# Performance work log

Measured on AMD Instinct MI355X. Metric: run time of the kernel, lower is better.

Reference implementation:

```python
import jax, jax.numpy as jnp
import numpy as np

DIM = 1024
S_SIZE = 512
M_SIZE = 4096
L_SIZE = 8192
MERGE_THRESHOLD = 0.98
L_ALPHA = 0.1
K_PROMOTE = max(1, S_SIZE // 4)  # torch: min(len(candidates), max(1, s_size//4)); candidates >> s_size here


def _l2norm(x, axis=-1):
    # F.normalize(p=2) with eps clamp
    return x / jnp.maximum(jnp.linalg.norm(x, axis=axis, keepdims=True), 1e-12)


def _update(processed_tokens, s_memory, m_memory, l_memory, m_utility, l_utility, wq, bq, wk, bk, s_ptr):
    cand = processed_tokens.reshape(-1, DIM)
    # --- S tier: scatter top-k-norm candidates into ring buffer (vectorized; K<=S so slots distinct) ---
    norms = jnp.linalg.norm(cand, axis=1)
    _, top_idx = jax.lax.top_k(norms, K_PROMOTE)
    pos = (s_ptr + jnp.arange(K_PROMOTE)) % S_SIZE
    s_mem = s_memory.at[pos].set(cand[top_idx])
    s_ptr_new = (s_ptr + K_PROMOTE) % S_SIZE
    # --- promotion attention (1 head, only attn weights used): pick best short-term slot ---
    q = l_memory.mean(axis=0) @ wq.T + bq                      # [dim]
    kproj = s_mem @ wk.T + bk                                  # [S, dim]
    attn = jax.nn.softmax(kproj @ q / jnp.sqrt(jnp.asarray(DIM, cand.dtype)))
    best_s_idx = jnp.argmax(attn)
    candidate = s_mem[best_s_idx]                              # [dim]

    # --- M tier: promote / merge / replace ---
    def not_full(mm, mu):
        ridx = jnp.argmin(mu)
        return mm.at[ridx].set(candidate), mu.at[ridx].set(mu.mean() + 1e-5)

    def full(mm, mu):
        mm_norm = _l2norm(mm)
        sims = mm_norm @ _l2norm(candidate)                    # [M]
        msi = jnp.argmax(sims)
        sim_cand = sims[msi]

        def merge_with_candidate(mm, mu):
            merged = _l2norm((mm[msi] + candidate) / 2.0)
            return mm.at[msi].set(merged), mu.at[msi].set((mu[msi] + mu.mean()) / 2.0)

        def try_internal_merge(mm, mu):
            # most redundant pair: strict lower triangle of cosine sim matrix
            sim_mat = mm_norm @ mm_norm.T                      # [M, M]
            sim_mat = jnp.where(jnp.triu(jnp.ones((M_SIZE, M_SIZE), bool)), -1.0, sim_mat)
            flat = jnp.argmax(sim_mat)
            internal_sim = sim_mat.reshape(-1)[flat]
            idx1, idx2 = flat // M_SIZE, flat % M_SIZE

            def do_pair_merge(mm, mu):
                merged = _l2norm((mm[idx1] + mm[idx2]) / 2.0)
                mm2 = mm.at[idx1].set(merged).at[idx2].set(candidate)
                mu1 = mu.at[idx1].set((mu[idx1] + mu[idx2]) / 2.0)
                mu2 = mu1.at[idx2].set(mu1.mean() + 1e-5)      # torch recomputes mean after idx1 write
                return mm2, mu2

            def replace_weakest(mm, mu):
                li = jnp.argmin(mu)
                stronger = jnp.linalg.norm(candidate) > jnp.linalg.norm(mm[li])
                mm2 = jnp.where(stronger, mm.at[li].set(candidate), mm)
                mu2 = jnp.where(stronger, mu.at[li].set(mu.mean() + 1e-5), mu)
                return mm2, mu2

            return jax.lax.cond(internal_sim > MERGE_THRESHOLD, do_pair_merge, replace_weakest, mm, mu)

        return jax.lax.cond(sim_cand > MERGE_THRESHOLD, merge_with_candidate, try_internal_merge, mm, mu)

    is_m_full = ~jnp.any(m_utility == 0)
    m_mem, m_util = jax.lax.cond(is_m_full, full, not_full, m_memory, m_utility)
    # --- L tier: consolidate most-used M slot into least-used L slot ---
    mi = jnp.argmax(m_util)
    lj = jnp.argmin(l_utility)
    consolidated = (1.0 - L_ALPHA) * l_memory[lj] + L_ALPHA * m_mem[mi]
    l_mem = l_memory.at[lj].set(consolidated)
    l_util = l_utility.at[lj].set(l_utility.mean())            # mean of pre-write values
    return s_mem, m_mem, l_mem, m_util, l_util, s_ptr_new


def setup_inputs() -> dict:
    key = jax.random.key(0)
    ks = jax.random.split(key, 10)
    scale = 1.0 / np.sqrt(DIM)
    return {
        "processed_tokens": jax.random.normal(ks[0], (4, 4096, DIM), jnp.float32),
        "s_memory": jax.random.normal(ks[1], (S_SIZE, DIM), jnp.float32),
        "m_memory": jax.random.normal(ks[2], (M_SIZE, DIM), jnp.float32),
        "l_memory": jax.random.normal(ks[3], (L_SIZE, DIM), jnp.float32),
        "m_utility": jax.random.uniform(ks[4], (M_SIZE,), jnp.float32) + 0.01,  # >0 -> 'm full' branch
        "l_utility": jax.random.uniform(ks[5], (L_SIZE,), jnp.float32) + 0.01,
        "wq": jax.random.normal(ks[6], (DIM, DIM), jnp.float32) * scale,
        "bq": jnp.zeros((DIM,), jnp.float32),
        "wk": jax.random.normal(ks[7], (DIM, DIM), jnp.float32) * scale,
        "bk": jnp.zeros((DIM,), jnp.float32),
        "s_ptr": 0,
    }


def reference(processed_tokens, s_memory, m_memory, l_memory, m_utility, l_utility, wq, bq, wk, bk, s_ptr):
    return _update(processed_tokens, s_memory, m_memory, l_memory, m_utility, l_utility, wq, bq, wk, bk, s_ptr)
```

## Files before the change

kernel.cpp:

```cpp
#include <hip/hip_runtime.h>

#define DIMV 1024
#define SSZ 512
#define MSZ 4096
#define LSZ 8192
#define KPROM 128
#define NCAND 16384
#define NPAIR 528

typedef __attribute__((ext_vector_type(4))) float f32x4;
typedef __attribute__((ext_vector_type(4))) unsigned int u32x4;
typedef __attribute__((ext_vector_type(4))) unsigned short u16x4;
typedef __attribute__((ext_vector_type(8))) __bf16 bf16x8;

#define OUT_S 0ull
#define OUT_M 524288ull
#define OUT_L 4718592ull
#define OUT_MU 13107200ull
#define OUT_LU 13111296ull
#define OUT_SPTR 13119488ull

#define SC_BF16 0ull
#define SC_NORMS 2100000ull
#define SC_TOPIDX 2117000ull
#define SC_LPART 2120000ull
#define SC_RV 2260000ull
#define SC_LMEAN 2262000ull
#define SC_Q 2264000ull
#define SC_LOGITS 2413000ull
#define SC_BEST 2414000ull
#define SC_MNORM 2415000ull
#define SC_SIMS 2420000ull
#define SC_PPV 2425000ull
#define SC_PPI 2427000ull

__device__ __forceinline__ float wave_sum(float v) {
#pragma unroll
  for (int o = 32; o > 0; o >>= 1) v += __shfl_down(v, o, 64);
  return v;
}
__device__ __forceinline__ void wave_maxidx(float& v, int& i) {
#pragma unroll
  for (int o = 32; o > 0; o >>= 1) {
    float ov = __shfl_down(v, o, 64);
    int oi = __shfl_down(i, o, 64);
    if (ov > v || (ov == v && oi < i)) { v = ov; i = oi; }
  }
}
__device__ __forceinline__ void wave_minidx(float& v, int& i) {
#pragma unroll
  for (int o = 32; o > 0; o >>= 1) {
    float ov = __shfl_down(v, o, 64);
    int oi = __shfl_down(i, o, 64);
    if (ov < v || (ov == v && oi < i)) { v = ov; i = oi; }
  }
}
__device__ __forceinline__ unsigned short f2bf(float x) {
  unsigned u = __float_as_uint(x);
  return (unsigned short)((u + 0x7FFFu + ((u >> 16) & 1u)) >> 16);
}
__device__ __forceinline__ void gload16(const unsigned short* g, unsigned short* l) {
  __builtin_amdgcn_global_load_lds((const __attribute__((address_space(1))) unsigned int*)(g),
                                   (__attribute__((address_space(3))) unsigned int*)(l), 16, 0, 0);
}

__global__ void kA(const float* __restrict__ cand, const float* __restrict__ l_memory,
                   const float* __restrict__ m, float* __restrict__ norms,
                   float* __restrict__ lpart, unsigned short* __restrict__ mb,
                   float* __restrict__ mnorm) {
  int b = blockIdx.x, t = threadIdx.x, lane = t & 63, w = t >> 6;
  if (b < 128) {
    f32x4 a0 = {0.f, 0.f, 0.f, 0.f}, a1 = a0, a2 = a0, a3 = a0;
    const f32x4* base = (const f32x4*)(l_memory + (size_t)b * 64 * DIMV);
#pragma unroll 4
    for (int r = 0; r < 64; r += 4) {
      a0 += base[(r + 0) * 256 + t];
      a1 += base[(r + 1) * 256 + t];
      a2 += base[(r + 2) * 256 + t];
      a3 += base[(r + 3) * 256 + t];
    }
    f32x4 a = (a0 + a1) + (a2 + a3);
    ((f32x4*)(lpart + (size_t)b * DIMV))[t] = a;
  } else if (b < 1152) {
    int r0 = (b - 128) * 16 + w * 4;
    const f32x4* base4 = (const f32x4*)(cand + (size_t)r0 * DIMV);
    float s0 = 0.f, s1 = 0.f, s2 = 0.f, s3 = 0.f;
#pragma unroll
    for (int k = 0; k < 16; ++k) {
      f32x4 v = base4[k * 64 + lane];
      float d = v.x * v.x + v.y * v.y + v.z * v.z + v.w * v.w;
      if (k < 4) s0 += d;
      else if (k < 8) s1 += d;
      else if (k < 12) s2 += d;
      else s3 += d;
    }
    f32x4 sv = {s0, s1, s2, s3};
#pragma unroll
    for (int o = 32; o > 0; o >>= 1) {
      sv.x += __shfl_down(sv.x, o, 64);
      sv.y += __shfl_down(sv.y, o, 64);
      sv.z += __shfl_down(sv.z, o, 64);
      sv.w += __shfl_down(sv.w, o, 64);
    }
    if (lane == 0) {
      f32x4 o4 = {sqrtf(sv.x), sqrtf(sv.y), sqrtf(sv.z), sqrtf(sv.w)};
      *((f32x4*)(norms + r0)) = o4;
    }
  } else {
    int r0 = (b - 1152) * 16 + w * 4;
    const f32x4* base4 = (const f32x4*)(m + (size_t)r0 * DIMV);
    u16x4* mb4 = (u16x4*)(mb + (size_t)r0 * DIMV);
    float s0 = 0.f, s1 = 0.f, s2 = 0.f, s3 = 0.f;
#pragma unroll
    for (int k = 0; k < 16; ++k) {
      int i = k * 64 + lane;
      f32x4 v = base4[i];
      float d = v.x * v.x + v.y * v.y + v.z * v.z + v.w * v.w;
      if (k < 4) s0 += d;
      else if (k < 8) s1 += d;
      else if (k < 12) s2 += d;
      else s3 += d;
      u16x4 h;
      h.x = f2bf(v.x); h.y = f2bf(v.y); h.z = f2bf(v.z); h.w = f2bf(v.w);
      mb4[i] = h;
    }
    f32x4 sv = {s0, s1, s2, s3};
#pragma unroll
    for (int o = 32; o > 0; o >>= 1) {
      sv.x += __shfl_down(sv.x, o, 64);
      sv.y += __shfl_down(sv.y, o, 64);
      sv.z += __shfl_down(sv.z, o, 64);
      sv.w += __shfl_down(sv.w, o, 64);
    }
    if (lane == 0) {
      f32x4 o4 = {sqrtf(sv.x), sqrtf(sv.y), sqrtf(sv.z), sqrtf(sv.w)};
      *((f32x4*)(mnorm + r0)) = o4;
    }
  }
}

__device__ int scan_excl_1024(int v, int* sh, int* total) {
  int t = threadIdx.x;
  sh[t] = v;
  __syncthreads();
  for (int o = 1; o < 1024; o <<= 1) {
    int x = (t >= o) ? sh[t - o] : 0;
    __syncthreads();
    sh[t] += x;
    __syncthreads();
  }
  int incl = sh[t];
  *total = sh[1023];
  __syncthreads();
  return incl - v;
}

__global__ void kT(const float* __restrict__ norms, int* __restrict__ topidx,
                   const float* __restrict__ lpart, float* __restrict__ lmean) {
  int t = threadIdx.x;
  if (blockIdx.x == 1) {
    float s = 0.f;
    for (int p = 0; p < 128; ++p) s += lpart[(size_t)p * DIMV + t];
    lmean[t] = s * (1.f / 8192.f);
    return;
  }
  __shared__ int sh[1024];
  __shared__ int hist[256];
  __shared__ unsigned s_selkey[KPROM];
  __shared__ int s_selidx[KPROM];
  __shared__ int s_digit, s_sub;
  unsigned key[16];
#pragma unroll
  for (int j = 0; j < 16; ++j) key[j] = __float_as_uint(norms[t * 16 + j]);

  unsigned prefix = 0, himask = 0;
  int remaining = KPROM;
  for (int p = 24; p >= 0; p -= 8) {
    if (t < 256) hist[t] = 0;
    __syncthreads();
#pragma unroll
    for (int j = 0; j < 16; ++j)
      if ((key[j] & himask) == prefix) atomicAdd(&hist[(key[j] >> p) & 255], 1);
    __syncthreads();
    if (t < 256) sh[t] = hist[t];
    __syncthreads();
    for (int o = 1; o < 256; o <<= 1) {
      int x = (t < 256 && t + o < 256) ? sh[t + o] : 0;
      __syncthreads();
      if (t < 256) sh[t] += x;
      __syncthreads();
    }
    if (t < 256) {
      int sfex = (t < 255) ? sh[t + 1] : 0;
      if (sfex < remaining && remaining <= sh[t]) { s_digit = t; s_sub = sfex; }
    }
    __syncthreads();
    prefix |= ((unsigned)s_digit) << p;
    remaining -= s_sub;
    himask |= (0xFFu << p);
    __syncthreads();
  }
  unsigned T = prefix;

  int cgt = 0, ceq = 0;
#pragma unroll
  for (int j = 0; j < 16; ++j) { cgt += (key[j] > T); ceq += (key[j] == T); }
  int total_gt, total_eq;
  int sgt = scan_excl_1024(cgt, sh, &total_gt);
  int seq = scan_excl_1024(ceq, sh, &total_eq);
  int need_eq = KPROM - total_gt;
  int g = sgt, e = seq;
#pragma unroll
  for (int j = 0; j < 16; ++j) {
    if (key[j] > T) { s_selkey[g] = key[j]; s_selidx[g] = t * 16 + j; ++g; }
    else if (key[j] == T) {
      if (e < need_eq) { s_selkey[total_gt + e] = key[j]; s_selidx[total_gt + e] = t * 16 + j; }
      ++e;
    }
  }
  __syncthreads();
  if (t < KPROM) {
    unsigned mk = s_selkey[t];
    int mi = s_selidx[t];
    int rank = 0;
    for (int q2 = 0; q2 < KPROM; ++q2) {
      unsigned qk = s_selkey[q2];
      int qi = s_selidx[q2];
      rank += (qk > mk || (qk == mk && qi < mi)) ? 1 : 0;
    }
    topidx[rank] = mi;
  }
}

__global__ void kB(const float* __restrict__ cand, const float* __restrict__ s_memory,
                   const int* __restrict__ topidx, const int* __restrict__ s_ptr,
                   const float* __restrict__ wq, const float* __restrict__ bq,
                   const float* __restrict__ lmean, float* __restrict__ out_s,
                   float* __restrict__ out_sptr, float* __restrict__ qv) {
  int b = blockIdx.x, t = threadIdx.x;
  if (b < 512) {
    int sp = s_ptr[0];
    int k = (b - sp + SSZ) & (SSZ - 1);
    const float* src = (k < KPROM) ? (cand + (size_t)topidx[k] * DIMV) : (s_memory + (size_t)b * DIMV);
    ((f32x4*)(out_s + (size_t)b * DIMV))[t] = ((const f32x4*)src)[t];
    if (b == 0 && t == 0) out_sptr[0] = (float)((sp + KPROM) % SSZ);
  } else {
    int lane = t & 63, w = t >> 6;
    int d = (b - 512) * 4 + w;
    const f32x4* row = (const f32x4*)(wq + (size_t)d * DIMV);
    const f32x4* lm = (const f32x4*)lmean;
    float s = 0.f;
#pragma unroll
    for (int c = 0; c < 4; ++c) {
      f32x4 a = row[c * 64 + lane], bb = lm[c * 64 + lane];
      s += a.x * bb.x + a.y * bb.y + a.z * bb.z + a.w * bb.w;
    }
    s = wave_sum(s);
    if (lane == 0) qv[d] = s + bq[d];
  }
}

__global__ void kC(const float* __restrict__ wk, const float* __restrict__ qv,
                   float* __restrict__ rv) {
  int b = blockIdx.x, t = threadIdx.x;
  f32x4 a = {0.f, 0.f, 0.f, 0.f};
  for (int r = 0; r < 8; ++r) {
    float qd = qv[b * 8 + r];
    f32x4 v = ((const f32x4*)(wk + (size_t)(b * 8 + r) * DIMV))[t];
    a += v * qd;
  }
  atomicAdd(&rv[t * 4 + 0], a.x);
  atomicAdd(&rv[t * 4 + 1], a.y);
  atomicAdd(&rv[t * 4 + 2], a.z);
  atomicAdd(&rv[t * 4 + 3], a.w);
}

__global__ void kD(const float* __restrict__ out_s, const float* __restrict__ rv,
                   float* __restrict__ logits) {
  int lane = threadIdx.x & 63, w = threadIdx.x >> 6;
  int srow = blockIdx.x * 4 + w;
  const f32x4* a = (const f32x4*)(out_s + (size_t)srow * DIMV);
  const f32x4* b = (const f32x4*)rv;
  float s = 0.f;
#pragma unroll
  for (int c = 0; c < 4; ++c) {
    f32x4 x = a[c * 64 + lane], y = b[c * 64 + lane];
    s += x.x * y.x + x.y * y.y + x.z * y.z + x.w * y.w;
  }
  s = wave_sum(s);
  if (lane == 0) logits[srow] = s;
}

__global__ void kE(const float* __restrict__ logits, const float* __restrict__ out_s,
                   int* __restrict__ best, float* __restrict__ cnorm) {
  __shared__ float swv[4];
  __shared__ int swi[4];
  int t = threadIdx.x, lane = t & 63, w = t >> 6;
  float v0 = logits[t], v1 = logits[t + 256];
  float bv;
  int bidx;
  if (v1 > v0) { bv = v1; bidx = t + 256; } else { bv = v0; bidx = t; }
  wave_maxidx(bv, bidx);
  if (lane == 0) { swv[w] = bv; swi[w] = bidx; }
  __syncthreads();
  if (t == 0) {
    float a = swv[0]; int ai = swi[0];
    for (int i = 1; i < 4; ++i)
      if (swv[i] > a || (swv[i] == a && swi[i] < ai)) { a = swv[i]; ai = swi[i]; }
    best[0] = ai;
  }
  __syncthreads();
  int bi = best[0];
  f32x4 c4 = ((const f32x4*)(out_s + (size_t)bi * DIMV))[t];
  float s = c4.x * c4.x + c4.y * c4.y + c4.z * c4.z + c4.w * c4.w;
  s = wave_sum(s);
  __syncthreads();
  if (lane == 0) swv[w] = s;
  __syncthreads();
  if (t == 0) cnorm[0] = sqrtf(swv[0] + swv[1] + swv[2] + swv[3]);
}

__global__ __launch_bounds__(256, 3) void kG(const unsigned short* __restrict__ mb,
                                             const float* __restrict__ mnorm,
                                             const float* __restrict__ m,
                                             const float* __restrict__ out_s,
                                             const int* __restrict__ best,
                                             const float* __restrict__ cnorm,
                                             float* __restrict__ pv, int* __restrict__ pidx,
                                             float* __restrict__ sims) {
  int b = blockIdx.x, t = threadIdx.x, lane = t & 63, w = t >> 6;
  if (b >= NPAIR) {
    int row = (b - NPAIR) * 4 + w;
    const f32x4* mp = (const f32x4*)(m + (size_t)row * DIMV);
    const f32x4* cp = (const f32x4*)(out_s + (size_t)best[0] * DIMV);
    float sd = 0.f;
#pragma unroll
    for (int c = 0; c < 4; ++c) {
      int i = c * 64 + lane;
      f32x4 v = mp[i], u = cp[i];
      sd += v.x * u.x + v.y * u.y + v.z * u.z + v.w * u.w;
    }
    sd = wave_sum(sd);
    if (lane == 0) sims[row] = sd / (fmaxf(mnorm[row], 1e-12f) * fmaxf(cnorm[0], 1e-12f));
    return;
  }
  __shared__ unsigned short Ash[128 * 64];
  __shared__ unsigned short Bsh[128 * 64];
  __shared__ float spv[4];
  __shared__ int spi[4];

  int bs = (b & 7) * 66 + (b >> 3);
  int bi = (int)((sqrtf(8.f * (float)bs + 1.f) - 1.f) * 0.5f);
  while (bi * (bi + 1) / 2 > bs) --bi;
  while ((bi + 1) * (bi + 2) / 2 <= bs) ++bi;
  int bj = bs - bi * (bi + 1) / 2;
  int rowA0 = bi * 128, rowB0 = bj * 128;

  int wr = w >> 1, wc = w & 1;
  int rl = lane & 15, kq4 = lane >> 4;
  int swz = rl & 7;
  int subrow = lane >> 3, gg = lane & 7;
  int gsw = (gg ^ subrow) << 3;

  f32x4 acc[4][4];
  f32x4 z = {0.f, 0.f, 0.f, 0.f};
#pragma unroll
  for (int ti = 0; ti < 4; ++ti)
#pragma unroll
    for (int tj = 0; tj < 4; ++tj) acc[ti][tj] = z;

  for (int kc = 0; kc < DIMV; kc += 64) {
#pragma unroll
    for (int jj = 0; jj < 4; ++jj) {
      int rsub = w * 32 + jj * 8 + subrow;
      gload16(mb + (size_t)(rowA0 + rsub) * DIMV + kc + gsw, Ash + (w * 4 + jj) * 512);
      gload16(mb + (size_t)(rowB0 + rsub) * DIMV + kc + gsw, Bsh + (w * 4 + jj) * 512);
    }
    __syncthreads();
#pragma unroll
    for (int ks = 0; ks < 2; ++ks) {
      int co = (((ks * 4 + kq4) ^ swz) << 3);
      bf16x8 af[4], bfv[4];
#pragma unroll
      for (int ti = 0; ti < 4; ++ti)
        af[ti] = *(const bf16x8*)(Ash + (wr * 64 + ti * 16 + rl) * 64 + co);
#pragma unroll
      for (int tj = 0; tj < 4; ++tj)
        bfv[tj] = *(const bf16x8*)(Bsh + (wc * 64 + tj * 16 + rl) * 64 + co);
#pragma unroll
      for (int ti = 0; ti < 4; ++ti)
#pragma unroll
        for (int tj = 0; tj < 4; ++tj)
          acc[ti][tj] = __builtin_amdgcn_mfma_f32_16x16x32_bf16(af[ti], bfv[tj], acc[ti][tj], 0, 0, 0);
    }
    __syncthreads();
  }

  float ni[16], nj4[4];
#pragma unroll
  for (int ti = 0; ti < 4; ++ti)
#pragma unroll
    for (int r = 0; r < 4; ++r)
      ni[ti * 4 + r] = fmaxf(mnorm[rowA0 + wr * 64 + ti * 16 + kq4 * 4 + r], 1e-12f);
#pragma unroll
  for (int tj = 0; tj < 4; ++tj)
    nj4[tj] = fmaxf(mnorm[rowB0 + wc * 64 + tj * 16 + rl], 1e-12f);

  float bv = -3.402823466e38f;
  int bidx = 0x7FFFFFFF;
#pragma unroll
  for (int ti = 0; ti < 4; ++ti)
#pragma unroll
    for (int tj = 0; tj < 4; ++tj)
#pragma unroll
      for (int r = 0; r < 4; ++r) {
        int gi = rowA0 + wr * 64 + ti * 16 + kq4 * 4 + r;
        int gj = rowB0 + wc * 64 + tj * 16 + rl;
        if (gi > gj) {
          float s = acc[ti][tj][r] / (ni[ti * 4 + r] * nj4[tj]);
          int fi = gi * MSZ + gj;
          if (s > bv || (s == bv && fi < bidx)) { bv = s; bidx = fi; }
        }
      }
  wave_maxidx(bv, bidx);
  if (lane == 0) { spv[w] = bv; spi[w] = bidx; }
  __syncthreads();
  if (t == 0) {
    float a = spv[0]; int ai = spi[0];
    for (int i = 1; i < 4; ++i)
      if (spv[i] > a || (spv[i] == a && spi[i] < ai)) { a = spv[i]; ai = spi[i]; }
    pv[b] = a;
    pidx[b] = ai;
  }
}

__global__ void kH(const float* __restrict__ pv, const int* __restrict__ pidx,
                   const float* __restrict__ sims, const float* __restrict__ mu,
                   const float* __restrict__ mnorm, const float* __restrict__ cnorm,
                   const int* __restrict__ best, const float* __restrict__ lu,
                   float* __restrict__ out_mu, float* __restrict__ out_lu,
                   int* __restrict__ ws) {
  __shared__ float swv[16];
  __shared__ int swi[16];
  __shared__ float ssum[16];
  __shared__ int szf[16];
  __shared__ float s_res[2];
  __shared__ int s_resi[2];
  __shared__ int s_branch, s_i1, s_i2, s_lj;
  __shared__ float s_u1, s_u2, s_lmean;
  int t = threadIdx.x, lane = t & 63, w = t >> 6;

  float bv = -3.402823466e38f;
  int bidx = 0x7FFFFFFF;
  for (int i = t; i < NPAIR; i += 1024) {
    float v = pv[i];
    int fi = pidx[i];
    if (v > bv || (v == bv && fi < bidx)) { bv = v; bidx = fi; }
  }
  wave_maxidx(bv, bidx);
  if (lane == 0) { swv[w] = bv; swi[w] = bidx; }
  __syncthreads();
  if (t == 0) {
    float a = swv[0]; int ai = swi[0];
    for (int i = 1; i < 16; ++i)
      if (swv[i] > a || (swv[i] == a && swi[i] < ai)) { a = swv[i]; ai = swi[i]; }
    s_res[0] = a; s_resi[0] = ai;
  }
  __syncthreads();

  bv = -3.402823466e38f;
  bidx = 0x7FFFFFFF;
#pragma unroll
  for (int j = 0; j < 4; ++j) {
    int i = t * 4 + j;
    float v = sims[i];
    if (v > bv) { bv = v; bidx = i; }
  }
  wave_maxidx(bv, bidx);
  if (lane == 0) { swv[w] = bv; swi[w] = bidx; }
  __syncthreads();
  if (t == 0) {
    float a = swv[0]; int ai = swi[0];
    for (int i = 1; i < 16; ++i)
      if (swv[i] > a || (swv[i] == a && swi[i] < ai)) { a = swv[i]; ai = swi[i]; }
    s_res[1] = a; s_resi[1] = ai;
  }
  __syncthreads();

  float muv[4];
  float sum = 0.f, mnv = 3.402823466e38f;
  int mni = 0x7FFFFFFF, zf = 0;
#pragma unroll
  for (int j = 0; j < 4; ++j) {
    int i = t * 4 + j;
    float v = mu[i];
    muv[j] = v;
    sum += v;
    if (v < mnv) { mnv = v; mni = i; }
    if (v == 0.f) zf = 1;
  }
  sum = wave_sum(sum);
  wave_minidx(mnv, mni);
#pragma unroll
  for (int o = 32; o > 0; o >>= 1) zf |= __shfl_down(zf, o, 64);
  if (lane == 0) { ssum[w] = sum; swv[w] = mnv; swi[w] = mni; szf[w] = zf; }
  __syncthreads();
  if (t == 0) {
    float muSum = 0.f;
    int anyz = 0;
    float a = swv[0]; int li = swi[0];
    for (int i = 0; i < 16; ++i) {
      muSum += ssum[i];
      anyz |= szf[i];
      if (i > 0 && (swv[i] < a || (swv[i] == a && swi[i] < li))) { a = swv[i]; li = swi[i]; }
    }
    float muMean = muSum / 4096.f;
    float internal_sim = s_res[0];
    int iflat = s_resi[0];
    float sim_cand = s_res[1];
    int msi = s_resi[1];
    int branch, i1 = -1, i2 = -1;
    float u1 = 0.f, u2 = 0.f;
    if (anyz) {
      branch = 0; i1 = li; u1 = muMean + 1e-5f;
    } else if (sim_cand > 0.98f) {
      branch = 1; i1 = msi; u1 = (mu[msi] + muMean) * 0.5f;
    } else if (internal_sim > 0.98f) {
      branch = 2; i1 = iflat / MSZ; i2 = iflat - (iflat / MSZ) * MSZ;
      float o1 = mu[i1], o2 = mu[i2];
      u1 = (o1 + o2) * 0.5f;
      u2 = (muSum - o1 + u1) / 4096.f + 1e-5f;
    } else {
      if (cnorm[0] > mnorm[li]) { branch = 0; i1 = li; u1 = muMean + 1e-5f; }
      else branch = 4;
    }
    s_branch = branch; s_i1 = i1; s_i2 = i2; s_u1 = u1; s_u2 = u2;
    ws[2] = branch; ws[3] = i1; ws[4] = i2; ws[5] = best[0];
  }
  __syncthreads();

  int branch = s_branch, i1 = s_i1, i2 = s_i2;
  float u1 = s_u1, u2 = s_u2;
  bv = -3.402823466e38f;
  bidx = 0x7FFFFFFF;
#pragma unroll
  for (int j = 0; j < 4; ++j) {
    int i = t * 4 + j;
    float v = muv[j];
    if (branch != 4 && i == i1) v = u1;
    if (branch == 2 && i == i2) v = u2;
    out_mu[i] = v;
    if (v > bv) { bv = v; bidx = i; }
  }
  wave_maxidx(bv, bidx);
  __syncthreads();
  if (lane == 0) { swv[w] = bv; swi[w] = bidx; }
  __syncthreads();
  if (t == 0) {
    float a = swv[0]; int ai = swi[0];
    for (int i = 1; i < 16; ++i)
      if (swv[i] > a || (swv[i] == a && swi[i] < ai)) { a = swv[i]; ai = swi[i]; }
    ws[1] = ai;
  }

  float luv[8];
  sum = 0.f; mnv = 3.402823466e38f; mni = 0x7FFFFFFF;
#pragma unroll
  for (int j = 0; j < 8; ++j) {
    int i = t * 8 + j;
    float v = lu[i];
    luv[j] = v;
    sum += v;
    if (v < mnv) { mnv = v; mni = i; }
  }
  sum = wave_sum(sum);
  wave_minidx(mnv, mni);
  __syncthreads();
  if (lane == 0) { swv[w] = mnv; swi[w] = mni; ssum[w] = sum; }
  __syncthreads();
  if (t == 0) {
    float a = swv[0]; int ai = swi[0];
    float ls = 0.f;
    for (int i = 0; i < 16; ++i) {
      ls += ssum[i];
      if (i > 0 && (swv[i] < a || (swv[i] == a && swi[i] < ai))) { a = swv[i]; ai = swi[i]; }
    }
    s_lj = ai;
    s_lmean = ls / 8192.f;
    ws[0] = ai;
  }
  __syncthreads();
  int lj = s_lj;
  float lmv = s_lmean;
#pragma unroll
  for (int j = 0; j < 8; ++j) {
    int i = t * 8 + j;
    out_lu[i] = (i == lj) ? lmv : luv[j];
  }
}

__global__ void kI(const float* __restrict__ m, const float* __restrict__ l_memory,
                   const float* __restrict__ out_s, const int* __restrict__ ws,
                   float* __restrict__ out_m, float* __restrict__ out_l) {
  __shared__ float sred[4];
  int b = blockIdx.x, t = threadIdx.x, lane = t & 63, w = t >> 6;
  int lj = ws[0], mi = ws[1], branch = ws[2], i1 = ws[3], i2 = ws[4], best = ws[5];
  if (b < 1024) {
    int r0 = b * 4;
    bool special = (branch != 4) &&
                   ((i1 >= r0 && i1 < r0 + 4) || (branch == 2 && i2 >= r0 && i2 < r0 + 4));
    if (!special) {
      const f32x4* src = (const f32x4*)(m + (size_t)r0 * DIMV);
      f32x4* dst = (f32x4*)(out_m + (size_t)r0 * DIMV);
#pragma unroll
      for (int k = 0; k < 4; ++k) dst[k * 256 + t] = src[k * 256 + t];
      return;
    }
    for (int rr = 0; rr < 4; ++rr) {
      int row = r0 + rr;
      int mode = 0;
      if ((branch == 0 && row == i1) || (branch == 2 && row == i2)) mode = 1;
      else if (branch == 1 && row == i1) mode = 2;
      else if (branch == 2 && row == i1) mode = 3;
      f32x4* dst = (f32x4*)(out_m + (size_t)row * DIMV);
      if (mode == 0) {
        dst[t] = ((const f32x4*)(m + (size_t)row * DIMV))[t];
      } else if (mode == 1) {
        dst[t] = ((const f32x4*)(out_s + (size_t)best * DIMV))[t];
      } else {
        f32x4 a = ((const f32x4*)(m + (size_t)row * DIMV))[t];
        f32x4 bb = (mode == 2) ? ((const f32x4*)(out_s + (size_t)best * DIMV))[t]
                               : ((const f32x4*)(m + (size_t)i2 * DIMV))[t];
        f32x4 v = (a + bb) * 0.5f;
        float ss = v.x * v.x + v.y * v.y + v.z * v.z + v.w * v.w;
        ss = wave_sum(ss);
        if (lane == 0) sred[w] = ss;
        __syncthreads();
        float nrm = fmaxf(sqrtf(sred[0] + sred[1] + sred[2] + sred[3]), 1e-12f);
        __syncthreads();
        dst[t] = v / nrm;
      }
    }
  } else {
    int r0 = (b - 1024) * 4;
    bool special = (lj >= r0 && lj < r0 + 4);
    if (!special) {
      const f32x4* src = (const f32x4*)(l_memory + (size_t)r0 * DIMV);
      f32x4* dst = (f32x4*)(out_l + (size_t)r0 * DIMV);
#pragma unroll
      for (int k = 0; k < 4; ++k) dst[k * 256 + t] = src[k * 256 + t];
      return;
    }
    for (int rr = 0; rr < 4; ++rr) {
      int row = r0 + rr;
      f32x4 v = ((const f32x4*)(l_memory + (size_t)row * DIMV))[t];
      if (row == lj) {
        int mode = 0;
        if ((branch == 0 && mi == i1) || (branch == 2 && mi == i2)) mode = 1;
        else if (branch == 1 && mi == i1) mode = 2;
        else if (branch == 2 && mi == i1) mode = 3;
        f32x4 mv;
        if (mode == 0) {
          mv = ((const f32x4*)(m + (size_t)mi * DIMV))[t];
        } else if (mode == 1) {
          mv = ((const f32x4*)(out_s + (size_t)best * DIMV))[t];
        } else {
          f32x4 a = ((const f32x4*)(m + (size_t)mi * DIMV))[t];
          f32x4 bb = (mode == 2) ? ((const f32x4*)(out_s + (size_t)best * DIMV))[t]
                                 : ((const f32x4*)(m + (size_t)i2 * DIMV))[t];
          f32x4 vm = (a + bb) * 0.5f;
          float ss = vm.x * vm.x + vm.y * vm.y + vm.z * vm.z + vm.w * vm.w;
          ss = wave_sum(ss);
          if (lane == 0) sred[w] = ss;
          __syncthreads();
          float nrm = fmaxf(sqrtf(sred[0] + sred[1] + sred[2] + sred[3]), 1e-12f);
          __syncthreads();
          mv = vm / nrm;
        }
        v = v * 0.9f + mv * 0.1f;
      }
      ((f32x4*)(out_l + (size_t)row * DIMV))[t] = v;
    }
  }
}

extern "C" void kernel_launch(void* const* d_in, const int* in_sizes, int n_in,
                              void* d_out, int out_size, void* d_ws, size_t ws_size,
                              hipStream_t stream) {
  const float* cand = (const float*)d_in[0];
  const float* s_memory = (const float*)d_in[1];
  const float* m_memory = (const float*)d_in[2];
  const float* l_memory = (const float*)d_in[3];
  const float* m_utility = (const float*)d_in[4];
  const float* l_utility = (const float*)d_in[5];
  const float* wq = (const float*)d_in[6];
  const float* bq = (const float*)d_in[7];
  const float* wk = (const float*)d_in[8];
  const float* bk = (const float*)d_in[9];
  const int* s_ptr = (const int*)d_in[10];
  (void)bk;

  float* out = (float*)d_out;
  float* out_s = out + OUT_S;
  float* out_m = out + OUT_M;
  float* out_l = out + OUT_L;
  float* out_mu = out + OUT_MU;
  float* out_lu = out + OUT_LU;
  float* out_sptr = out + OUT_SPTR;

  float* lsc = out_l;
  unsigned short* mb = (unsigned short*)(lsc + SC_BF16);
  float* norms = lsc + SC_NORMS;
  int* topidx = (int*)(lsc + SC_TOPIDX);
  float* lpart = lsc + SC_LPART;
  float* rv = lsc + SC_RV;
  float* lmean = lsc + SC_LMEAN;
  float* qv = lsc + SC_Q;
  float* logits = lsc + SC_LOGITS;
  int* best = (int*)(lsc + SC_BEST);
  float* cnorm = lsc + SC_BEST + 1;
  float* mnorm = lsc + SC_MNORM;
  float* sims = lsc + SC_SIMS;
  float* pv = lsc + SC_PPV;
  int* pidx = (int*)(lsc + SC_PPI);
  int* wsctl = (int*)d_ws;

  hipMemsetAsync(rv, 0, 4096, stream);
  kA<<<1408, 256, 0, stream>>>(cand, l_memory, m_memory, norms, lpart, mb, mnorm);
  kT<<<2, 1024, 0, stream>>>(norms, topidx, lpart, lmean);
  kB<<<768, 256, 0, stream>>>(cand, s_memory, topidx, s_ptr, wq, bq, lmean, out_s, out_sptr, qv);
  kC<<<128, 256, 0, stream>>>(wk, qv, rv);
  kD<<<128, 256, 0, stream>>>(out_s, rv, logits);
  kE<<<1, 256, 0, stream>>>(logits, out_s, best, cnorm);
  kG<<<NPAIR + 1024, 256, 0, stream>>>(mb, mnorm, m_memory, out_s, best, cnorm, pv, pidx, sims);
  kH<<<1, 1024, 0, stream>>>(pv, pidx, sims, m_utility, mnorm, cnorm, best, l_utility,
                             out_mu, out_lu, wsctl);
  kI<<<3072, 256, 0, stream>>>(m_memory, l_memory, out_s, wsctl, out_m, out_l);
}
```

Before: 284.0 us.

## Fuse M/L passthrough copies into first streaming pass with nontemporal stores

```diff
diff --git a/kernel.cpp b/kernel.cpp
--- a/kernel.cpp
+++ b/kernel.cpp
@@ -20,19 +20,19 @@
 #define OUT_LU 13111296ull
 #define OUT_SPTR 13119488ull
 
+#define SCROWS 2080
 #define SC_BF16 0ull
-#define SC_NORMS 2100000ull
-#define SC_TOPIDX 2117000ull
-#define SC_LPART 2120000ull
-#define SC_RV 2260000ull
-#define SC_LMEAN 2262000ull
-#define SC_Q 2264000ull
-#define SC_LOGITS 2413000ull
-#define SC_BEST 2414000ull
-#define SC_MNORM 2415000ull
-#define SC_SIMS 2420000ull
-#define SC_PPV 2425000ull
-#define SC_PPI 2427000ull
+#define SC_NORMS 2097152ull
+#define SC_TOPIDX 2113536ull
+#define SC_RV 2113664ull
+#define SC_LSUM 2114688ull
+#define SC_QV 2115712ull
+#define SC_LOGITS 2116736ull
+#define SC_BEST 2117248ull
+#define SC_MNORM 2117264ull
+#define SC_SIMS 2121360ull
+#define SC_PPV 2125456ull
+#define SC_PPI 2125984ull
 
 __device__ __forceinline__ float wave_sum(float v) {
 #pragma unroll
@@ -59,6 +59,7 @@
   unsigned u = __float_as_uint(x);
   return (unsigned short)((u + 0x7FFFu + ((u >> 16) & 1u)) >> 16);
 }
+__device__ __forceinline__ void nts(f32x4* p, f32x4 v) { __builtin_nontemporal_store(v, p); }
 __device__ __forceinline__ void gload16(const unsigned short* g, unsigned short* l) {
   __builtin_amdgcn_global_load_lds((const __attribute__((address_space(1))) unsigned int*)(g),
                                    (__attribute__((address_space(3))) unsigned int*)(l), 16, 0, 0);
@@ -66,50 +67,40 @@
 
 __global__ void kA(const float* __restrict__ cand, const float* __restrict__ l_memory,
                    const float* __restrict__ m, float* __restrict__ norms,
-                   float* __restrict__ lpart, unsigned short* __restrict__ mb,
-                   float* __restrict__ mnorm) {
+                   float* __restrict__ lsum, unsigned short* __restrict__ mb,
+                   float* __restrict__ mnorm, float* __restrict__ out_m,
+                   float* __restrict__ out_l) {
   int b = blockIdx.x, t = threadIdx.x, lane = t & 63, w = t >> 6;
-  if (b < 128) {
+  if (b < 256) {
+    int r0 = b * 32;
+    const f32x4* base = (const f32x4*)l_memory + (size_t)r0 * 256;
+    f32x4* dst = (f32x4*)out_l + (size_t)r0 * 256;
+    bool wr = (r0 >= SCROWS);
     f32x4 a0 = {0.f, 0.f, 0.f, 0.f}, a1 = a0, a2 = a0, a3 = a0;
-    const f32x4* base = (const f32x4*)(l_memory + (size_t)b * 64 * DIMV);
-#pragma unroll 4
-    for (int r = 0; r < 64; r += 4) {
-      a0 += base[(r + 0) * 256 + t];
-      a1 += base[(r + 1) * 256 + t];
-      a2 += base[(r + 2) * 256 + t];
-      a3 += base[(r + 3) * 256 + t];
+#pragma unroll 2
+    for (int r = 0; r < 32; r += 4) {
+      f32x4 v0 = base[(r + 0) * 256 + t];
+      f32x4 v1 = base[(r + 1) * 256 + t];
+      f32x4 v2 = base[(r + 2) * 256 + t];
+      f32x4 v3 = base[(r + 3) * 256 + t];
+      if (wr) {
+        nts(&dst[(r + 0) * 256 + t], v0);
+        nts(&dst[(r + 1) * 256 + t], v1);
+        nts(&dst[(r + 2) * 256 + t], v2);
+        nts(&dst[(r + 3) * 256 + t], v3);
+      }
+      a0 += v0; a1 += v1; a2 += v2; a3 += v3;
     }
     f32x4 a = (a0 + a1) + (a2 + a3);
-    ((f32x4*)(lpart + (size_t)b * DIMV))[t] = a;
-  } else if (b < 1152) {
-    int r0 = (b - 128) * 16 + w * 4;
-    const f32x4* base4 = (const f32x4*)(cand + (size_t)r0 * DIMV);
-    float s0 = 0.f, s1 = 0.f, s2 = 0.f, s3 = 0.f;
-#pragma unroll
-    for (int k = 0; k < 16; ++k) {
-      f32x4 v = base4[k * 64 + lane];
-      float d = v.x * v.x + v.y * v.y + v.z * v.z + v.w * v.w;
-      if (k < 4) s0 += d;
-      else if (k < 8) s1 += d;
-      else if (k < 12) s2 += d;
-      else s3 += d;
-    }
-    f32x4 sv = {s0, s1, s2, s3};
-#pragma unroll
-    for (int o = 32; o > 0; o >>= 1) {
-      sv.x += __shfl_down(sv.x, o, 64);
-      sv.y += __shfl_down(sv.y, o, 64);
-      sv.z += __shfl_down(sv.z, o, 64);
-      sv.w += __shfl_down(sv.w, o, 64);
-    }
-    if (lane == 0) {
-      f32x4 o4 = {sqrtf(sv.x), sqrtf(sv.y), sqrtf(sv.z), sqrtf(sv.w)};
-      *((f32x4*)(norms + r0)) = o4;
-    }
-  } else {
-    int r0 = (b - 1152) * 16 + w * 4;
+    atomicAdd(&lsum[t * 4 + 0], a.x);
+    atomicAdd(&lsum[t * 4 + 1], a.y);
+    atomicAdd(&lsum[t * 4 + 2], a.z);
+    atomicAdd(&lsum[t * 4 + 3], a.w);
+  } else if (b < 512) {
+    int r0 = (b - 256) * 16 + w * 4;
     const f32x4* base4 = (const f32x4*)(m + (size_t)r0 * DIMV);
     u16x4* mb4 = (u16x4*)(mb + (size_t)r0 * DIMV);
+    f32x4* om4 = (f32x4*)(out_m + (size_t)r0 * DIMV);
     float s0 = 0.f, s1 = 0.f, s2 = 0.f, s3 = 0.f;
 #pragma unroll
     for (int k = 0; k < 16; ++k) {
@@ -123,6 +114,7 @@
       u16x4 h;
       h.x = f2bf(v.x); h.y = f2bf(v.y); h.z = f2bf(v.z); h.w = f2bf(v.w);
       mb4[i] = h;
+      nts(&om4[i], v);
     }
     f32x4 sv = {s0, s1, s2, s3};
 #pragma unroll
@@ -136,6 +128,31 @@
       f32x4 o4 = {sqrtf(sv.x), sqrtf(sv.y), sqrtf(sv.z), sqrtf(sv.w)};
       *((f32x4*)(mnorm + r0)) = o4;
     }
+  } else {
+    int r0 = (b - 512) * 16 + w * 4;
+    const f32x4* base4 = (const f32x4*)(cand + (size_t)r0 * DIMV);
+    float s0 = 0.f, s1 = 0.f, s2 = 0.f, s3 = 0.f;
+#pragma unroll
+    for (int k = 0; k < 16; ++k) {
+      f32x4 v = base4[k * 64 + lane];
+      float d = v.x * v.x + v.y * v.y + v.z * v.z + v.w * v.w;
+      if (k < 4) s0 += d;
+      else if (k < 8) s1 += d;
+      else if (k < 12) s2 += d;
+      else s3 += d;
+    }
+    f32x4 sv = {s0, s1, s2, s3};
+#pragma unroll
+    for (int o = 32; o > 0; o >>= 1) {
+      sv.x += __shfl_down(sv.x, o, 64);
+      sv.y += __shfl_down(sv.y, o, 64);
+      sv.z += __shfl_down(sv.z, o, 64);
+      sv.w += __shfl_down(sv.w, o, 64);
+    }
+    if (lane == 0) {
+      f32x4 o4 = {sqrtf(sv.x), sqrtf(sv.y), sqrtf(sv.z), sqrtf(sv.w)};
+      *((f32x4*)(norms + r0)) = o4;
+    }
   }
 }
 
@@ -155,23 +172,22 @@
   return incl - v;
 }
 
-__global__ void kT(const float* __restrict__ norms, int* __restrict__ topidx,
-                   const float* __restrict__ lpart, float* __restrict__ lmean) {
+__global__ void kT(const float* __restrict__ norms, int* __restrict__ topidx) {
   int t = threadIdx.x;
-  if (blockIdx.x == 1) {
-    float s = 0.f;
-    for (int p = 0; p < 128; ++p) s += lpart[(size_t)p * DIMV + t];
-    lmean[t] = s * (1.f / 8192.f);
-    return;
-  }
   __shared__ int sh[1024];
   __shared__ int hist[256];
   __shared__ unsigned s_selkey[KPROM];
   __shared__ int s_selidx[KPROM];
   __shared__ int s_digit, s_sub;
   unsigned key[16];
-#pragma unroll
-  for (int j = 0; j < 16; ++j) key[j] = __float_as_uint(norms[t * 16 + j]);
+  {
+    const u32x4* np = (const u32x4*)norms;
+    u32x4 k0 = np[t * 4 + 0], k1 = np[t * 4 + 1], k2 = np[t * 4 + 2], k3 = np[t * 4 + 3];
+    key[0] = k0.x; key[1] = k0.y; key[2] = k0.z; key[3] = k0.w;
+    key[4] = k1.x; key[5] = k1.y; key[6] = k1.z; key[7] = k1.w;
+    key[8] = k2.x; key[9] = k2.y; key[10] = k2.z; key[11] = k2.w;
+    key[12] = k3.x; key[13] = k3.y; key[14] = k3.z; key[15] = k3.w;
+  }
 
   unsigned prefix = 0, himask = 0;
   int remaining = KPROM;
@@ -235,7 +251,7 @@
 __global__ void kB(const float* __restrict__ cand, const float* __restrict__ s_memory,
                    const int* __restrict__ topidx, const int* __restrict__ s_ptr,
                    const float* __restrict__ wq, const float* __restrict__ bq,
-                   const float* __restrict__ lmean, float* __restrict__ out_s,
+                   const float* __restrict__ lsum, float* __restrict__ out_s,
                    float* __restrict__ out_sptr, float* __restrict__ qv) {
   int b = blockIdx.x, t = threadIdx.x;
   if (b < 512) {
@@ -248,7 +264,7 @@
     int lane = t & 63, w = t >> 6;
     int d = (b - 512) * 4 + w;
     const f32x4* row = (const f32x4*)(wq + (size_t)d * DIMV);
-    const f32x4* lm = (const f32x4*)lmean;
+    const f32x4* lm = (const f32x4*)lsum;
     float s = 0.f;
 #pragma unroll
     for (int c = 0; c < 4; ++c) {
@@ -256,7 +272,7 @@
       s += a.x * bb.x + a.y * bb.y + a.z * bb.z + a.w * bb.w;
     }
     s = wave_sum(s);
-    if (lane == 0) qv[d] = s + bq[d];
+    if (lane == 0) qv[d] = s * (1.f / 8192.f) + bq[d];
   }
 }
 
@@ -605,83 +621,66 @@
   __shared__ float sred[4];
   int b = blockIdx.x, t = threadIdx.x, lane = t & 63, w = t >> 6;
   int lj = ws[0], mi = ws[1], branch = ws[2], i1 = ws[3], i2 = ws[4], best = ws[5];
-  if (b < 1024) {
+  if (b < 520) {
     int r0 = b * 4;
-    bool special = (branch != 4) &&
-                   ((i1 >= r0 && i1 < r0 + 4) || (branch == 2 && i2 >= r0 && i2 < r0 + 4));
-    if (!special) {
-      const f32x4* src = (const f32x4*)(m + (size_t)r0 * DIMV);
-      f32x4* dst = (f32x4*)(out_m + (size_t)r0 * DIMV);
-#pragma unroll
-      for (int k = 0; k < 4; ++k) dst[k * 256 + t] = src[k * 256 + t];
-      return;
-    }
-    for (int rr = 0; rr < 4; ++rr) {
-      int row = r0 + rr;
-      int mode = 0;
-      if ((branch == 0 && row == i1) || (branch == 2 && row == i2)) mode = 1;
-      else if (branch == 1 && row == i1) mode = 2;
-      else if (branch == 2 && row == i1) mode = 3;
-      f32x4* dst = (f32x4*)(out_m + (size_t)row * DIMV);
-      if (mode == 0) {
-        dst[t] = ((const f32x4*)(m + (size_t)row * DIMV))[t];
-      } else if (mode == 1) {
-        dst[t] = ((const f32x4*)(out_s + (size_t)best * DIMV))[t];
-      } else {
-        f32x4 a = ((const f32x4*)(m + (size_t)row * DIMV))[t];
-        f32x4 bb = (mode == 2) ? ((const f32x4*)(out_s + (size_t)best * DIMV))[t]
+    const f32x4* src = (const f32x4*)(l_memory + (size_t)r0 * DIMV);
+    f32x4* dst = (f32x4*)(out_l + (size_t)r0 * DIMV);
+#pragma unroll
+    for (int k = 0; k < 4; ++k) {
+      if (r0 + k == lj) continue;
+      nts(&dst[k * 256 + t], src[k * 256 + t]);
+    }
+    return;
+  }
+  if (b == 520) {
+    if (branch == 4) return;
+    int row = i1;
+    f32x4* dst = (f32x4*)(out_m + (size_t)row * DIMV);
+    if (branch == 0) {
+      dst[t] = ((const f32x4*)(out_s + (size_t)best * DIMV))[t];
+    } else {
+      f32x4 a = ((const f32x4*)(m + (size_t)row * DIMV))[t];
+      f32x4 bb = (branch == 1) ? ((const f32x4*)(out_s + (size_t)best * DIMV))[t]
                                : ((const f32x4*)(m + (size_t)i2 * DIMV))[t];
-        f32x4 v = (a + bb) * 0.5f;
-        float ss = v.x * v.x + v.y * v.y + v.z * v.z + v.w * v.w;
-        ss = wave_sum(ss);
-        if (lane == 0) sred[w] = ss;
-        __syncthreads();
-        float nrm = fmaxf(sqrtf(sred[0] + sred[1] + sred[2] + sred[3]), 1e-12f);
-        __syncthreads();
-        dst[t] = v / nrm;
-      }
-    }
+      f32x4 v = (a + bb) * 0.5f;
+      float ss = v.x * v.x + v.y * v.y + v.z * v.z + v.w * v.w;
+      ss = wave_sum(ss);
+      if (lane == 0) sred[w] = ss;
+      __syncthreads();
+      float nrm = fmaxf(sqrtf(sred[0] + sred[1] + sred[2] + sred[3]), 1e-12f);
+      dst[t] = v / nrm;
+    }
+    return;
+  }
+  if (b == 521) {
+    if (branch != 2) return;
+    ((f32x4*)(out_m + (size_t)i2 * DIMV))[t] = ((const f32x4*)(out_s + (size_t)best * DIMV))[t];
+    return;
+  }
+  f32x4 v = ((const f32x4*)(l_memory + (size_t)lj * DIMV))[t];
+  int mode = 0;
+  if ((branch == 0 && mi == i1) || (branch == 2 && mi == i2)) mode = 1;
+  else if (branch == 1 && mi == i1) mode = 2;
+  else if (branch == 2 && mi == i1) mode = 3;
+  f32x4 mv;
+  if (mode == 0) {
+    mv = ((const f32x4*)(m + (size_t)mi * DIMV))[t];
+  } else if (mode == 1) {
+    mv = ((const f32x4*)(out_s + (size_t)best * DIMV))[t];
   } else {
-    int r0 = (b - 1024) * 4;
-    bool special = (lj >= r0 && lj < r0 + 4);
-    if (!special) {
-      const f32x4* src = (const f32x4*)(l_memory + (size_t)r0 * DIMV);
-      f32x4* dst = (f32x4*)(out_l + (size_t)r0 * DIMV);
-#pragma unroll
-      for (int k = 0; k < 4; ++k) dst[k * 256 + t] = src[k * 256 + t];
-      return;
-    }
-    for (int rr = 0; rr < 4; ++rr) {
-      int row = r0 + rr;
-      f32x4 v = ((const f32x4*)(l_memory + (size_t)row * DIMV))[t];
-      if (row == lj) {
-        int mode = 0;
-        if ((branch == 0 && mi == i1) || (branch == 2 && mi == i2)) mode = 1;
-        else if (branch == 1 && mi == i1) mode = 2;
-        else if (branch == 2 && mi == i1) mode = 3;
-        f32x4 mv;
-        if (mode == 0) {
-          mv = ((const f32x4*)(m + (size_t)mi * DIMV))[t];
-        } else if (mode == 1) {
-          mv = ((const f32x4*)(out_s + (size_t)best * DIMV))[t];
-        } else {
-          f32x4 a = ((const f32x4*)(m + (size_t)mi * DIMV))[t];
-          f32x4 bb = (mode == 2) ? ((const f32x4*)(out_s + (size_t)best * DIMV))[t]
-                                 : ((const f32x4*)(m + (size_t)i2 * DIMV))[t];
-          f32x4 vm = (a + bb) * 0.5f;
-          float ss = vm.x * vm.x + vm.y * vm.y + vm.z * vm.z + vm.w * vm.w;
-          ss = wave_sum(ss);
-          if (lane == 0) sred[w] = ss;
-          __syncthreads();
-          float nrm = fmaxf(sqrtf(sred[0] + sred[1] + sred[2] + sred[3]), 1e-12f);
-          __syncthreads();
-          mv = vm / nrm;
-        }
-        v = v * 0.9f + mv * 0.1f;
-      }
-      ((f32x4*)(out_l + (size_t)row * DIMV))[t] = v;
-    }
-  }
+    f32x4 a = ((const f32x4*)(m + (size_t)mi * DIMV))[t];
+    f32x4 bb = (mode == 2) ? ((const f32x4*)(out_s + (size_t)best * DIMV))[t]
+                           : ((const f32x4*)(m + (size_t)i2 * DIMV))[t];
+    f32x4 vm = (a + bb) * 0.5f;
+    float ss = vm.x * vm.x + vm.y * vm.y + vm.z * vm.z + vm.w * vm.w;
+    ss = wave_sum(ss);
+    if (lane == 0) sred[w] = ss;
+    __syncthreads();
+    float nrm = fmaxf(sqrtf(sred[0] + sred[1] + sred[2] + sred[3]), 1e-12f);
+    mv = vm / nrm;
+  }
+  v = v * 0.9f + mv * 0.1f;
+  ((f32x4*)(out_l + (size_t)lj * DIMV))[t] = v;
 }
 
 extern "C" void kernel_launch(void* const* d_in, const int* in_sizes, int n_in,
@@ -712,10 +711,9 @@
   unsigned short* mb = (unsigned short*)(lsc + SC_BF16);
   float* norms = lsc + SC_NORMS;
   int* topidx = (int*)(lsc + SC_TOPIDX);
-  float* lpart = lsc + SC_LPART;
   float* rv = lsc + SC_RV;
-  float* lmean = lsc + SC_LMEAN;
-  float* qv = lsc + SC_Q;
+  float* lsum = lsc + SC_LSUM;
+  float* qv = lsc + SC_QV;
   float* logits = lsc + SC_LOGITS;
   int* best = (int*)(lsc + SC_BEST);
   float* cnorm = lsc + SC_BEST + 1;
@@ -725,15 +723,15 @@
   int* pidx = (int*)(lsc + SC_PPI);
   int* wsctl = (int*)d_ws;
 
-  hipMemsetAsync(rv, 0, 4096, stream);
-  kA<<<1408, 256, 0, stream>>>(cand, l_memory, m_memory, norms, lpart, mb, mnorm);
-  kT<<<2, 1024, 0, stream>>>(norms, topidx, lpart, lmean);
-  kB<<<768, 256, 0, stream>>>(cand, s_memory, topidx, s_ptr, wq, bq, lmean, out_s, out_sptr, qv);
+  hipMemsetAsync(rv, 0, 8192, stream);
+  kA<<<1536, 256, 0, stream>>>(cand, l_memory, m_memory, norms, lsum, mb, mnorm, out_m, out_l);
+  kT<<<1, 1024, 0, stream>>>(norms, topidx);
+  kB<<<768, 256, 0, stream>>>(cand, s_memory, topidx, s_ptr, wq, bq, lsum, out_s, out_sptr, qv);
   kC<<<128, 256, 0, stream>>>(wk, qv, rv);
   kD<<<128, 256, 0, stream>>>(out_s, rv, logits);
   kE<<<1, 256, 0, stream>>>(logits, out_s, best, cnorm);
   kG<<<NPAIR + 1024, 256, 0, stream>>>(mb, mnorm, m_memory, out_s, best, cnorm, pv, pidx, sims);
   kH<<<1, 1024, 0, stream>>>(pv, pidx, sims, m_utility, mnorm, cnorm, best, l_utility,
                              out_mu, out_lu, wsctl);
-  kI<<<3072, 256, 0, stream>>>(m_memory, l_memory, out_s, wsctl, out_m, out_l);
-}
+  kI<<<523, 256, 0, stream>>>(m_memory, l_memory, out_s, wsctl, out_m, out_l);
+}
```

Result: slower. 294.2 us (+3.6%).
